# Performance work log

Measured on AMD Instinct MI355X. Metric: run time of the kernel, lower is better.

## Reference

```python
import jax, jax.numpy as jnp
import numpy as np

B, D_IMG, D_TXT, E = 4096, 768, 768, 512
LAMBDA_CMP = 1.0
EPS = 1e-10


def setup_inputs() -> dict:
    key = jax.random.key(0)
    k1, k2, k3, k4, k5 = jax.random.split(key, 5)
    return {
        "images": jax.random.normal(k1, (B, D_IMG), dtype=jnp.float32),
        "texts": jax.random.normal(k2, (B, D_TXT), dtype=jnp.float32),
        "labels": jax.random.randint(k3, (B,), 0, 1000, dtype=jnp.int32),
        "W_img": jax.random.normal(k4, (D_IMG, E), dtype=jnp.float32) / np.sqrt(D_IMG),
        "W_txt": jax.random.normal(k5, (D_TXT, E), dtype=jnp.float32) / np.sqrt(D_TXT),
        "logit_scale": jnp.asarray(np.log(1.0 / 0.07), dtype=jnp.float32),
    }


def reference(images, texts, labels, W_img, W_txt, logit_scale):
    # CLIP-style encoders: linear project + L2 normalize
    img = images @ W_img
    txt = texts @ W_txt
    img = img / jnp.linalg.norm(img, axis=-1, keepdims=True)
    txt = txt / jnp.linalg.norm(txt, axis=-1, keepdims=True)
    logits = jnp.exp(logit_scale) * (img @ txt.T)  # [B, B]

    b = logits.shape[0]
    rows = jnp.arange(b)
    logp = jax.nn.log_softmax(logits, axis=-1)
    clip_loss = -jnp.mean(logp[rows, labels])

    probs = jnp.exp(logp)                # softmax probs [B, B]
    p_yi = probs[rows, labels]           # [B]
    # columns j whose label differs from sample i's label AND prob exceeds p_yi
    diff_label = labels[None, :] != labels[:, None]           # [B, B]
    mask = diff_label & (probs > p_yi[:, None])               # [B, B]
    denom = jnp.sum(jnp.where(mask, probs, 0.0), axis=1)      # [B]
    has_any = jnp.any(mask, axis=1)
    cmp_loss = jnp.sum(jnp.where(has_any, p_yi / (denom + EPS), 0.0)) / b

    return clip_loss + LAMBDA_CMP * cmp_loss
```

## Files before the change

kernel.cpp:

```cpp
#include <hip/hip_runtime.h>
#include <stdint.h>

#define BATCH 4096
#define DDIM  768
#define EDIM  512
#define NSPLIT 64
#define LOG2E 1.44269504088896340736f

using short8  = __attribute__((ext_vector_type(8))) short;
using float4v = __attribute__((ext_vector_type(4))) float;

__device__ __forceinline__ unsigned short f2bf(float x) {
    union { float f; uint32_t u; } v; v.f = x;
    uint32_t u = v.u;
    u += 0x7FFFu + ((u >> 16) & 1u);
    return (unsigned short)(u >> 16);
}
__device__ __forceinline__ float bf2f(unsigned short h) {
    union { uint32_t u; float f; } v; v.u = ((uint32_t)h) << 16;
    return v.f;
}

__device__ __forceinline__ void gl2lds16(const void* g, void* l) {
    __builtin_amdgcn_global_load_lds(
        (const __attribute__((address_space(1))) void*)g,
        (__attribute__((address_space(3))) void*)l, 16, 0, 0);
}

__global__ void cvt2(const float* __restrict__ a, const float* __restrict__ b,
                     unsigned short* __restrict__ oa, unsigned short* __restrict__ ob) {
    int i = blockIdx.x * 256 + threadIdx.x;
    const float* in = blockIdx.y ? b : a;
    unsigned short* out = blockIdx.y ? ob : oa;
    float4 v = ((const float4*)in)[i];
    ushort4 o;
    o.x = f2bf(v.x); o.y = f2bf(v.y); o.z = f2bf(v.z); o.w = f2bf(v.w);
    ((ushort4*)out)[i] = o;
}

__global__ void transpose2(const float* __restrict__ Wa, const float* __restrict__ Wb,
                           unsigned short* __restrict__ Ta, unsigned short* __restrict__ Tb) {
    const float* W = blockIdx.z ? Wb : Wa;
    unsigned short* Wt = blockIdx.z ? Tb : Ta;
    __shared__ float tile[32][33];
    int n0 = blockIdx.x * 32, k0 = blockIdx.y * 32;
    int tid = threadIdx.x;
    for (int p = 0; p < 4; ++p) {
        int e = tid + p * 256; int lr = e >> 5, lc = e & 31;
        tile[lc][lr] = W[(size_t)(k0 + lr) * EDIM + n0 + lc];
    }
    __syncthreads();
    for (int p = 0; p < 4; ++p) {
        int e = tid + p * 256; int lr = e >> 5, lc = e & 31;
        Wt[(size_t)(n0 + lr) * DDIM + k0 + lc] = f2bf(tile[lr][lc]);
    }
}

__global__ __launch_bounds__(256) void gemm_nt(const unsigned short* __restrict__ Aimg,
                                               const unsigned short* __restrict__ Atxt,
                                               const unsigned short* __restrict__ Bimg,
                                               const unsigned short* __restrict__ Btxt,
                                               unsigned short* __restrict__ Cimg,
                                               unsigned short* __restrict__ Ctxt) {
    const unsigned short* A  = blockIdx.z ? Atxt : Aimg;
    const unsigned short* Bm = blockIdx.z ? Btxt : Bimg;
    unsigned short* C        = blockIdx.z ? Ctxt : Cimg;
    __shared__ __align__(16) unsigned short As[2 * 128 * 32];
    __shared__ __align__(16) unsigned short Bs[2 * 64 * 32];
    int tid = threadIdx.x;
    int wave = tid >> 6, lane = tid & 63;
    int q = lane >> 4, r = lane & 15;
    int m0 = blockIdx.x * 128, n0 = blockIdx.y * 64;
    int sw = (r >> 1) & 3;

    const unsigned short* gsA[4];
    unsigned short* lsA[4];
    for (int i = 0; i < 4; ++i) {
        int u = i * 256 + tid;
        int kc2 = u >> 9, row = (u >> 2) & 127, kq = u & 3;
        int kq2 = kq ^ ((row >> 1) & 3);
        gsA[i] = &A[(size_t)(m0 + row) * DDIM + kc2 * 32 + kq2 * 8];
        lsA[i] = &As[u * 8];
    }
    const unsigned short* gsB[2];
    unsigned short* lsB[2];
    for (int i = 0; i < 2; ++i) {
        int u = i * 256 + tid;
        int kc2 = u >> 8, row = (u >> 2) & 63, kq = u & 3;
        int kq2 = kq ^ ((row >> 1) & 3);
        gsB[i] = &Bm[(size_t)(n0 + row) * DDIM + kc2 * 32 + kq2 * 8];
        lsB[i] = &Bs[u * 8];
    }

    float4v acc[2][4];
    for (int a = 0; a < 2; ++a)
        for (int t = 0; t < 4; ++t) acc[a][t] = (float4v){0.f, 0.f, 0.f, 0.f};

    for (int it = 0; it < DDIM / 64; ++it) {
        int k0 = it * 64;
        __syncthreads();
        for (int i = 0; i < 4; ++i) gl2lds16(gsA[i] + k0, lsA[i]);
        for (int i = 0; i < 2; ++i) gl2lds16(gsB[i] + k0, lsB[i]);
        __syncthreads();
        for (int kc2 = 0; kc2 < 2; ++kc2) {
            short8 a0 = *(const short8*)&As[kc2 * 4096 + (wave * 32 + r) * 32 + (q ^ sw) * 8];
            short8 a1 = *(const short8*)&As[kc2 * 4096 + (wave * 32 + 16 + r) * 32 + (q ^ sw) * 8];
            for (int t = 0; t < 4; ++t) {
                short8 b = *(const short8*)&Bs[kc2 * 2048 + (t * 16 + r) * 32 + (q ^ sw) * 8];
                acc[0][t] = __builtin_amdgcn_mfma_f32_16x16x32_bf16(a0, b, acc[0][t], 0, 0, 0);
                acc[1][t] = __builtin_amdgcn_mfma_f32_16x16x32_bf16(a1, b, acc[1][t], 0, 0, 0);
            }
        }
    }
    for (int rg = 0; rg < 2; ++rg)
        for (int t = 0; t < 4; ++t)
            for (int g = 0; g < 4; ++g)
                C[(size_t)(m0 + wave * 32 + rg * 16 + q * 4 + g) * EDIM + n0 + t * 16 + r] =
                    f2bf(acc[rg][t][g]);
}

__global__ void norm_rows(unsigned short* __restrict__ Pa, unsigned short* __restrict__ Pb) {
    unsigned short* P = blockIdx.y ? Pb : Pa;
    int wave = threadIdx.x >> 6, lane = threadIdx.x & 63;
    int row = blockIdx.x * 4 + wave;
    unsigned short* p = &P[(size_t)row * 512 + lane * 8];
    union { unsigned short us[8]; uint4 u4; } v;
    v.u4 = *(const uint4*)p;
    float f[8], s = 0.f;
    for (int j = 0; j < 8; ++j) { f[j] = bf2f(v.us[j]); s += f[j] * f[j]; }
    for (int off = 1; off < 64; off <<= 1) s += __shfl_xor(s, off);
    float rn = rsqrtf(s);
    for (int j = 0; j < 8; ++j) v.us[j] = f2bf(f[j] * rn);
    *(uint4*)p = v.u4;
}

__global__ void tdot(const unsigned short* __restrict__ img, const unsigned short* __restrict__ txt,
                     const int* __restrict__ labels, float* __restrict__ tout) {
    int wave = threadIdx.x >> 6, lane = threadIdx.x & 63;
    int row = blockIdx.x * 4 + wave;
    int lab = labels[row];
    union { unsigned short us[8]; uint4 u4; } a, b;
    a.u4 = *(const uint4*)&img[(size_t)row * 512 + lane * 8];
    b.u4 = *(const uint4*)&txt[(size_t)lab * 512 + lane * 8];
    float s = 0.f;
    for (int j = 0; j < 8; ++j) s += bf2f(a.us[j]) * bf2f(b.us[j]);
    for (int off = 1; off < 64; off <<= 1) s += __shfl_xor(s, off);
    if (lane == 0) tout[row] = s;
}

__global__ __launch_bounds__(256) void flash_pass(
    const unsigned short* __restrict__ img, const unsigned short* __restrict__ txt,
    const int* __restrict__ labels, const float* __restrict__ tvals,
    const float* __restrict__ ls,
    float* __restrict__ lP, float* __restrict__ dP) {
    __shared__ __align__(16) unsigned short Bs[16 * 64 * 32];
    int tid = threadIdx.x;
    int wave = tid >> 6, lane = tid & 63;
    int q = lane >> 4, r = lane & 15;
    int row0 = blockIdx.x * 128 + wave * 32;
    int split = blockIdx.y;
    int colbase = split * 64;
    float alpha = expf(ls[0]);
    float c1 = alpha * LOG2E;

    int srow = tid >> 2, skp = tid & 3;
    int skp2 = skp ^ ((srow >> 1) & 3);
    int sw = (r >> 1) & 3;

    const unsigned short* gB = &txt[(size_t)(colbase + srow) * 512 + skp2 * 8];
    for (int i = 0; i < 16; ++i)
        gl2lds16(gB + i * 32, &Bs[i * 2048 + tid * 8]);

    short8 af[2][16];
    for (int rg = 0; rg < 2; ++rg)
        for (int kc = 0; kc < 16; ++kc)
            af[rg][kc] = *(const short8*)&img[(size_t)(row0 + rg * 16 + r) * 512 + kc * 32 + q * 8];

    int labr[8]; float tr[8];
    for (int rg = 0; rg < 2; ++rg)
        for (int g = 0; g < 4; ++g) {
            int rw = row0 + rg * 16 + q * 4 + g;
            labr[rg * 4 + g] = labels[rw];
            tr[rg * 4 + g] = tvals[rw];
        }
    int lc[4];
    for (int t = 0; t < 4; ++t) lc[t] = labels[colbase + t * 16 + r];

    float4v acc[2][4];
    for (int rg = 0; rg < 2; ++rg)
        for (int t = 0; t < 4; ++t) acc[rg][t] = (float4v){0.f, 0.f, 0.f, 0.f};

    __syncthreads();

    for (int kc = 0; kc < 16; ++kc) {
        short8 a0 = af[0][kc];
        short8 a1 = af[1][kc];
        for (int t = 0; t < 4; ++t) {
            short8 bf = *(const short8*)&Bs[(kc * 64 + t * 16 + r) * 32 + (q ^ sw) * 8];
            acc[0][t] = __builtin_amdgcn_mfma_f32_16x16x32_bf16(a0, bf, acc[0][t], 0, 0, 0);
            acc[1][t] = __builtin_amdgcn_mfma_f32_16x16x32_bf16(a1, bf, acc[1][t], 0, 0, 0);
        }
    }

    float l[8] = {0.f}, d[8] = {0.f};
    for (int t = 0; t < 4; ++t)
        for (int rg = 0; rg < 2; ++rg)
            for (int g = 0; g < 4; ++g) {
                float a = acc[rg][t][g];
                float p = exp2f(fmaf(a, c1, -c1));
                int ix = rg * 4 + g;
                l[ix] += p;
                d[ix] += ((a > tr[ix]) && (lc[t] != labr[ix])) ? p : 0.f;
            }

    for (int ix = 0; ix < 8; ++ix) {
        float lv = l[ix], dv = d[ix];
        for (int off = 1; off < 16; off <<= 1) {
            lv += __shfl_xor(lv, off);
            dv += __shfl_xor(dv, off);
        }
        if (r == 0) {
            int rw = row0 + (ix >> 2) * 16 + q * 4 + (ix & 3);
            lP[(size_t)split * BATCH + rw] = lv;
            dP[(size_t)split * BATCH + rw] = dv;
        }
    }
}

__global__ void combine(const float* __restrict__ lP, const float* __restrict__ dP,
                        const float* __restrict__ tvals, const float* __restrict__ ls,
                        float* __restrict__ out) {
    int row = blockIdx.x * 256 + threadIdx.x;
    float alpha = expf(ls[0]);
    float L = 0.f, D = 0.f;
    for (int s = 0; s < NSPLIT; ++s) {
        L += lP[(size_t)s * BATCH + row];
        D += dP[(size_t)s * BATCH + row];
    }
    float tm = alpha * (tvals[row] - 1.0f);
    float clip = logf(L) - tm;
    float py = expf(tm) / L;
    float cmp = (D > 0.f) ? py / (D / L + 1e-10f) : 0.f;
    float v = clip + cmp;
    for (int off = 1; off < 64; off <<= 1) v += __shfl_xor(v, off);
    __shared__ float w4[4];
    int wave = threadIdx.x >> 6, lane = threadIdx.x & 63;
    if (lane == 0) w4[wave] = v;
    __syncthreads();
    if (threadIdx.x == 0)
        atomicAdd(out, (w4[0] + w4[1] + w4[2] + w4[3]) * (1.0f / BATCH));
}

extern "C" void kernel_launch(void* const* d_in, const int* in_sizes, int n_in,
                              void* d_out, int out_size, void* d_ws, size_t ws_size,
                              hipStream_t stream) {
    const float* images = (const float*)d_in[0];
    const float* texts  = (const float*)d_in[1];
    const int*   labels = (const int*)d_in[2];
    const float* W_img  = (const float*)d_in[3];
    const float* W_txt  = (const float*)d_in[4];
    const float* lscale = (const float*)d_in[5];
    float* out = (float*)d_out;

    char* ws = (char*)d_ws;
    unsigned short* img_bf = (unsigned short*)(ws + 0);
    unsigned short* txt_bf = (unsigned short*)(ws + 6291456);
    unsigned short* wt_img = (unsigned short*)(ws + 12582912);
    unsigned short* wt_txt = (unsigned short*)(ws + 13369344);
    unsigned short* proj_i = (unsigned short*)(ws + 14155776);
    unsigned short* proj_t = (unsigned short*)(ws + 18350080);
    float*          lP     = (float*)(ws + 0);
    float*          dP     = (float*)(ws + 1048576);
    float*          tvals  = (float*)(ws + 2097152);

    hipMemsetAsync(out, 0, sizeof(float), stream);
    cvt2<<<dim3(3072, 2), 256, 0, stream>>>(images, texts, img_bf, txt_bf);
    transpose2<<<dim3(EDIM / 32, DDIM / 32, 2), 256, 0, stream>>>(W_img, W_txt, wt_img, wt_txt);
    gemm_nt<<<dim3(BATCH / 128, EDIM / 64, 2), 256, 0, stream>>>(img_bf, txt_bf, wt_img, wt_txt,
                                                                 proj_i, proj_t);
    norm_rows<<<dim3(BATCH / 4, 2), 256, 0, stream>>>(proj_i, proj_t);
    tdot<<<BATCH / 4, 256, 0, stream>>>(proj_i, proj_t, labels, tvals);
    flash_pass<<<dim3(BATCH / 128, NSPLIT), 256, 0, stream>>>(proj_i, proj_t, labels, tvals, lscale,
                                                              lP, dP);
    combine<<<16, 256, 0, stream>>>(lP, dP, tvals, lscale, out);
}
```

Measured before the change: 155.7 us.

## Retile flash pass to 128x128 block tiles with staged K loop in LDS

The logits kernel now computes a 128x128 output tile per block, with a 2x2 wave layout where each wave owns a 64x64 subtile. A and B are streamed through LDS in K-chunks of 32 instead of keeping the A rows in registers and the whole B slab in LDS. Each loaded fragment now feeds more MFMAs, which cuts global and LDS traffic per FLOP. The price is two barriers per K step with no double buffering, so load latency sits exposed. NSPLIT stays at 64 because split is blockIdx.y*2+wn.

```diff
diff --git a/kernel.cpp b/kernel.cpp
--- a/kernel.cpp
+++ b/kernel.cpp
@@ -153,76 +153,80 @@
     const int* __restrict__ labels, const float* __restrict__ tvals,
     const float* __restrict__ ls,
     float* __restrict__ lP, float* __restrict__ dP) {
-    __shared__ __align__(16) unsigned short Bs[16 * 64 * 32];
+    __shared__ __align__(16) unsigned short As[128 * 32];
+    __shared__ __align__(16) unsigned short Bs[128 * 32];
     int tid = threadIdx.x;
     int wave = tid >> 6, lane = tid & 63;
+    int wm = wave >> 1, wn = wave & 1;
     int q = lane >> 4, r = lane & 15;
-    int row0 = blockIdx.x * 128 + wave * 32;
-    int split = blockIdx.y;
-    int colbase = split * 64;
-    float alpha = expf(ls[0]);
-    float c1 = alpha * LOG2E;
-
-    int srow = tid >> 2, skp = tid & 3;
-    int skp2 = skp ^ ((srow >> 1) & 3);
+    int row0 = blockIdx.x * 128, col0 = blockIdx.y * 128;
+    float c1 = expf(ls[0]) * LOG2E;
+
     int sw = (r >> 1) & 3;
-
-    const unsigned short* gB = &txt[(size_t)(colbase + srow) * 512 + skp2 * 8];
-    for (int i = 0; i < 16; ++i)
-        gl2lds16(gB + i * 32, &Bs[i * 2048 + tid * 8]);
-
-    short8 af[2][16];
-    for (int rg = 0; rg < 2; ++rg)
-        for (int kc = 0; kc < 16; ++kc)
-            af[rg][kc] = *(const short8*)&img[(size_t)(row0 + rg * 16 + r) * 512 + kc * 32 + q * 8];
-
-    int labr[8]; float tr[8];
-    for (int rg = 0; rg < 2; ++rg)
+    const unsigned short* gsA[2]; unsigned short* lsA[2];
+    const unsigned short* gsB[2]; unsigned short* lsB[2];
+    for (int i = 0; i < 2; ++i) {
+        int c = i * 256 + tid;
+        int row = c >> 2, kq = c & 3;
+        int kq2 = kq ^ ((row >> 1) & 3);
+        gsA[i] = &img[(size_t)(row0 + row) * 512 + kq2 * 8];
+        lsA[i] = &As[c * 8];
+        gsB[i] = &txt[(size_t)(col0 + row) * 512 + kq2 * 8];
+        lsB[i] = &Bs[c * 8];
+    }
+
+    float4v acc[4][4];
+    #pragma unroll
+    for (int i = 0; i < 4; ++i)
+        for (int t = 0; t < 4; ++t) acc[i][t] = (float4v){0.f, 0.f, 0.f, 0.f};
+
+    for (int it = 0; it < 16; ++it) {
+        int k0 = it * 32;
+        __syncthreads();
+        gl2lds16(gsA[0] + k0, lsA[0]); gl2lds16(gsA[1] + k0, lsA[1]);
+        gl2lds16(gsB[0] + k0, lsB[0]); gl2lds16(gsB[1] + k0, lsB[1]);
+        __syncthreads();
+        short8 a[4], b[4];
+        #pragma unroll
+        for (int i = 0; i < 4; ++i)
+            a[i] = *(const short8*)&As[(wm * 64 + i * 16 + r) * 32 + (q ^ sw) * 8];
+        #pragma unroll
+        for (int t = 0; t < 4; ++t)
+            b[t] = *(const short8*)&Bs[(wn * 64 + t * 16 + r) * 32 + (q ^ sw) * 8];
+        #pragma unroll
+        for (int i = 0; i < 4; ++i)
+            #pragma unroll
+            for (int t = 0; t < 4; ++t)
+                acc[i][t] = __builtin_amdgcn_mfma_f32_16x16x32_bf16(a[i], b[t], acc[i][t], 0, 0, 0);
+    }
+
+    int lc[4];
+    #pragma unroll
+    for (int t = 0; t < 4; ++t) lc[t] = labels[col0 + wn * 64 + t * 16 + r];
+    int split = blockIdx.y * 2 + wn;
+    #pragma unroll
+    for (int i = 0; i < 4; ++i) {
+        #pragma unroll
         for (int g = 0; g < 4; ++g) {
-            int rw = row0 + rg * 16 + q * 4 + g;
-            labr[rg * 4 + g] = labels[rw];
-            tr[rg * 4 + g] = tvals[rw];
-        }
-    int lc[4];
-    for (int t = 0; t < 4; ++t) lc[t] = labels[colbase + t * 16 + r];
-
-    float4v acc[2][4];
-    for (int rg = 0; rg < 2; ++rg)
-        for (int t = 0; t < 4; ++t) acc[rg][t] = (float4v){0.f, 0.f, 0.f, 0.f};
-
-    __syncthreads();
-
-    for (int kc = 0; kc < 16; ++kc) {
-        short8 a0 = af[0][kc];
-        short8 a1 = af[1][kc];
-        for (int t = 0; t < 4; ++t) {
-            short8 bf = *(const short8*)&Bs[(kc * 64 + t * 16 + r) * 32 + (q ^ sw) * 8];
-            acc[0][t] = __builtin_amdgcn_mfma_f32_16x16x32_bf16(a0, bf, acc[0][t], 0, 0, 0);
-            acc[1][t] = __builtin_amdgcn_mfma_f32_16x16x32_bf16(a1, bf, acc[1][t], 0, 0, 0);
-        }
-    }
-
-    float l[8] = {0.f}, d[8] = {0.f};
-    for (int t = 0; t < 4; ++t)
-        for (int rg = 0; rg < 2; ++rg)
-            for (int g = 0; g < 4; ++g) {
-                float a = acc[rg][t][g];
-                float p = exp2f(fmaf(a, c1, -c1));
-                int ix = rg * 4 + g;
-                l[ix] += p;
-                d[ix] += ((a > tr[ix]) && (lc[t] != labr[ix])) ? p : 0.f;
-            }
-
-    for (int ix = 0; ix < 8; ++ix) {
-        float lv = l[ix], dv = d[ix];
-        for (int off = 1; off < 16; off <<= 1) {
-            lv += __shfl_xor(lv, off);
-            dv += __shfl_xor(dv, off);
-        }
-        if (r == 0) {
-            int rw = row0 + (ix >> 2) * 16 + q * 4 + (ix & 3);
-            lP[(size_t)split * BATCH + rw] = lv;
-            dP[(size_t)split * BATCH + rw] = dv;
+            int rw = row0 + wm * 64 + i * 16 + q * 4 + g;
+            int lr = labels[rw];
+            float tv = tvals[rw];
+            float pl = 0.f, pd = 0.f;
+            #pragma unroll
+            for (int t = 0; t < 4; ++t) {
+                float av = acc[i][t][g];
+                float p = exp2f(fmaf(av, c1, -c1));
+                pl += p;
+                pd += ((av > tv) && (lc[t] != lr)) ? p : 0.f;
+            }
+            for (int off = 1; off < 16; off <<= 1) {
+                pl += __shfl_xor(pl, off);
+                pd += __shfl_xor(pd, off);
+            }
+            if (r == 0) {
+                lP[(size_t)split * BATCH + rw] = pl;
+                dP[(size_t)split * BATCH + rw] = pd;
+            }
         }
     }
 }
@@ -280,7 +284,7 @@
                                                                  proj_i, proj_t);
     norm_rows<<<dim3(BATCH / 4, 2), 256, 0, stream>>>(proj_i, proj_t);
     tdot<<<BATCH / 4, 256, 0, stream>>>(proj_i, proj_t, labels, tvals);
-    flash_pass<<<dim3(BATCH / 128, NSPLIT), 256, 0, stream>>>(proj_i, proj_t, labels, tvals, lscale,
-                                                              lP, dP);
+    flash_pass<<<dim3(BATCH / 128, BATCH / 128), 256, 0, stream>>>(proj_i, proj_t, labels, tvals,
+                                                                   lscale, lP, dP);
     combine<<<16, 256, 0, stream>>>(lP, dP, tvals, lscale, out);
 }
```

New measurement: 142.3 us. -8.6%, faster.
